# Kernel tuning notes

Hardware: AMD Instinct MI355X
Metric: run time of the kernel (lower is better)

## Reference

```python
import jax, jax.numpy as jnp
import numpy as np

B, H, T = 32, 48, 24
S, A, R, F, L = 256, 64, 8, 1024, 2
EPS = 1e-5


def setup_inputs() -> dict:
    key = jax.random.key(0)
    ks = jax.random.split(key, 12)
    def w(k, shape):
        fan_in = shape[-1]
        return jax.random.normal(k, shape, jnp.float32) / jnp.sqrt(jnp.float32(fan_in))
    return {
        'history_s': jax.random.normal(ks[0], (B, H, S), jnp.float32),
        'history_a': jax.random.normal(ks[1], (B, H, A), jnp.float32),
        'present_s': jax.random.normal(ks[2], (B, S), jnp.float32),
        'future_s': jax.random.normal(ks[3], (B, T, S), jnp.float32),
        'future_a': jax.random.normal(ks[4], (B, T, A), jnp.float32),
        'W_state': w(ks[5], (F, S)), 'b_state': jnp.zeros((F,), jnp.float32),
        'g_sn': jnp.ones((F,), jnp.float32), 'b_sn': jnp.zeros((F,), jnp.float32),
        'W_action': w(ks[6], (F, A)), 'b_action': jnp.zeros((F,), jnp.float32),
        'g_an': jnp.ones((F,), jnp.float32), 'b_an': jnp.zeros((F,), jnp.float32),
        'gru_Wi': w(ks[7], (L, 3 * F, F)), 'gru_Wh': w(ks[8], (L, 3 * F, F)),
        'gru_bi': jnp.zeros((L, 3 * F), jnp.float32), 'gru_bh': jnp.zeros((L, 3 * F), jnp.float32),
        'W_reward': w(ks[9], (R, F)), 'b_reward': jnp.zeros((R,), jnp.float32),
        'W_sout': w(ks[10], (S, F)), 'b_sout': jnp.zeros((S,), jnp.float32),
    }


def _ln(x, g, b):
    m = jnp.mean(x, axis=-1, keepdims=True)
    v = jnp.mean(jnp.square(x - m), axis=-1, keepdims=True)
    return (x - m) / jnp.sqrt(v + EPS) * g + b


def _gelu(x):
    return jax.nn.gelu(x, approximate=False)  # torch F.gelu default = exact erf


def _gru_step(Wi, Wh, bi, bh, hs, x):
    # hs: [L,B,F] hidden per layer; x: [B,F]. PyTorch GRU cell semantics.
    new_hs = []
    inp = x
    for l in range(Wi.shape[0]):
        gi = inp @ Wi[l].T + bi[l]      # [B,3F]
        gh = hs[l] @ Wh[l].T + bh[l]    # [B,3F]
        ir, iz, inn = jnp.split(gi, 3, axis=-1)
        hr, hz, hn = jnp.split(gh, 3, axis=-1)
        r = jax.nn.sigmoid(ir + hr)
        z = jax.nn.sigmoid(iz + hz)
        n = jnp.tanh(inn + r * hn)
        h_new = (1.0 - z) * n + z * hs[l]
        new_hs.append(h_new)
        inp = h_new  # dropout between layers is identity (drop_rate=0)
    return jnp.stack(new_hs), inp


def reference(history_s, history_a, present_s, future_s, future_a,
              W_state, b_state, g_sn, b_sn, W_action, b_action, g_an, b_an,
              gru_Wi, gru_Wh, gru_bi, gru_bh, W_reward, b_reward, W_sout, b_sout):
    # Original forward() reruns the GRU from scratch over a growing window each
    # future step; since h0=0 this is mathematically identical to carrying the
    # hidden state incrementally (module's own _forward variant), which we do.
    Bv = history_s.shape[0]
    Fv = W_state.shape[0]
    Lv = gru_Wi.shape[0]

    hs = _ln(history_s @ W_state.T + b_state, g_sn, b_sn)   # [B,H,F]
    ha = _ln(history_a @ W_action.T + b_action, g_an, b_an)  # [B,H,F]
    ps = _ln(present_s @ W_state.T + b_state, g_sn, b_sn)    # [B,F]
    fa = _ln(future_a @ W_action.T + b_action, g_an, b_an)   # [B,T,F]

    hist_sa = hs + ha  # [B,H,F]

    def head(y):
        r = jnp.tanh(y @ W_reward.T + b_reward)
        s = y @ W_sout.T + b_sout  # state_activation is identity
        return r, s

    # step 0: full window = history + (present + future_a[0])
    seq0 = _gelu(jnp.concatenate([hist_sa, (ps + fa[:, 0])[:, None, :]], axis=1))
    h0 = jnp.zeros((Lv, Bv, Fv), seq0.dtype)

    def scan_seq(h, x):
        h, y = _gru_step(gru_Wi, gru_Wh, gru_bi, gru_bh, h, x)
        return h, y

    hT, ys = jax.lax.scan(scan_seq, h0, jnp.swapaxes(seq0, 0, 1))  # ys: [H+1,B,F]
    r0, s0 = head(ys[-1])
    pres = _ln(s0 @ W_state.T + b_state, g_sn, b_sn)

    def scan_fut(carry, fa_t):
        h, p = carry
        x = _gelu(p + fa_t)  # [B,F]
        h, y = _gru_step(gru_Wi, gru_Wh, gru_bi, gru_bh, h, x)
        r, s = head(y)
        p_new = _ln(s @ W_state.T + b_state, g_sn, b_sn)
        return (h, p_new), (r, s)

    _, (rs, ss) = jax.lax.scan(scan_fut, (hT, pres), jnp.swapaxes(fa[:, 1:], 0, 1))
    future_r = jnp.concatenate([r0[:, None], jnp.swapaxes(rs, 0, 1)], axis=1)  # [B,T,R]
    future_s_out = jnp.concatenate([s0[:, None], jnp.swapaxes(ss, 0, 1)], axis=1)  # [B,T,S]
    return future_r, future_s_out
```

## Files before the change

### kernel.cpp

```cpp
#include <hip/hip_runtime.h>
#include <cmath>

constexpr int kB = 32, kH = 48, kT = 24, kS = 256, kA = 64, kR = 8, kF = 1024;
constexpr int kSEQ = kH + 1;
constexpr float kEPS = 1e-5f;

constexpr int G  = 128;
constexpr int BT = 512;

typedef __attribute__((ext_vector_type(8))) short short8;
typedef __attribute__((ext_vector_type(4))) float f32x4;

union U4S8 { uint4 u; short8 s; };

__device__ __forceinline__ unsigned bfbits(float x) {
  unsigned u = __float_as_uint(x);
  return (u + 0x7fffu + ((u >> 16) & 1u)) >> 16;
}
__device__ __forceinline__ float bf_lo(unsigned u) { return __uint_as_float(u << 16); }
__device__ __forceinline__ float bf_hi(unsigned u) { return __uint_as_float(u & 0xffff0000u); }
__device__ __forceinline__ float bf2f(unsigned short h) {
  return __uint_as_float(((unsigned)h) << 16);
}
__device__ __forceinline__ float gelu_f(float x) {
  return 0.5f * x * (1.0f + erff(x * 0.7071067811865476f));
}
__device__ __forceinline__ float sigmoid_f(float x) {
  return 1.0f / (1.0f + expf(-x));
}

__device__ __forceinline__ void coh_st(unsigned* p, unsigned v) {
  __hip_atomic_store(p, v, __ATOMIC_RELAXED, __HIP_MEMORY_SCOPE_AGENT);
}

__device__ __forceinline__ void sig(unsigned* fl, int grp) {
  if (threadIdx.x == 0)
    __hip_atomic_fetch_add(fl + (grp & 3) * 32, 1u,
                           __ATOMIC_RELAXED, __HIP_MEMORY_SCOPE_AGENT);
}
__device__ __forceinline__ void wait4(const unsigned* fl,
                                      unsigned t0, unsigned t1,
                                      unsigned t2, unsigned t3) {
  if (threadIdx.x == 0) {
    for (;;) {
      unsigned a, b, c, d;
      asm volatile(
        "global_load_dword %0, %4, off sc0 sc1\n\t"
        "global_load_dword %1, %5, off sc0 sc1\n\t"
        "global_load_dword %2, %6, off sc0 sc1\n\t"
        "global_load_dword %3, %7, off sc0 sc1\n\t"
        "s_waitcnt vmcnt(0)"
        : "=&v"(a), "=&v"(b), "=&v"(c), "=&v"(d)
        : "v"(fl), "v"(fl + 32), "v"(fl + 64), "v"(fl + 96)
        : "memory");
      if (a >= t0 && b >= t1 && c >= t2 && d >= t3) break;
    }
  }
  __syncthreads();
}

__device__ __forceinline__ void layer_stage(
    const unsigned short* __restrict__ xsrc,
    const unsigned short* __restrict__ hsrc,
    unsigned short* __restrict__ hdst,
    const short8 (&Bf)[2][3][4],
    float bR, float bZ, float bIN, float bHN,
    float& h_old, float* part, int fb)
{
  const int tid = threadIdx.x;
  const int wv = tid >> 6, l = tid & 63, q = l >> 4, c = l & 15;

  short8 Afr[2][2][4];
  #pragma unroll
  for (int mt = 0; mt < 2; mt++)
    #pragma unroll
    for (int j = 0; j < 4; j++) {
      const int off = (mt*16 + c)*1024 + wv*128 + j*32 + q*8;
      Afr[0][mt][j] = *(const short8*)(xsrc + off);
      Afr[1][mt][j] = *(const short8*)(hsrc + off);
    }

  f32x4 C[4][2];
  #pragma unroll
  for (int s = 0; s < 4; s++)
    #pragma unroll
    for (int mt = 0; mt < 2; mt++)
      C[s][mt] = (f32x4){0.f, 0.f, 0.f, 0.f};

  #pragma unroll
  for (int mt = 0; mt < 2; mt++)
    #pragma unroll
    for (int j = 0; j < 4; j++) {
      C[0][mt] = __builtin_amdgcn_mfma_f32_16x16x32_bf16(Afr[0][mt][j], Bf[0][0][j], C[0][mt], 0, 0, 0);
      C[0][mt] = __builtin_amdgcn_mfma_f32_16x16x32_bf16(Afr[1][mt][j], Bf[1][0][j], C[0][mt], 0, 0, 0);
      C[1][mt] = __builtin_amdgcn_mfma_f32_16x16x32_bf16(Afr[0][mt][j], Bf[0][1][j], C[1][mt], 0, 0, 0);
      C[1][mt] = __builtin_amdgcn_mfma_f32_16x16x32_bf16(Afr[1][mt][j], Bf[1][1][j], C[1][mt], 0, 0, 0);
      C[2][mt] = __builtin_amdgcn_mfma_f32_16x16x32_bf16(Afr[0][mt][j], Bf[0][2][j], C[2][mt], 0, 0, 0);
      C[3][mt] = __builtin_amdgcn_mfma_f32_16x16x32_bf16(Afr[1][mt][j], Bf[1][2][j], C[3][mt], 0, 0, 0);
    }

  const int perm = (wv + l + (l >> 3)) & 7;
  #pragma unroll
  for (int s = 0; s < 4; s++)
    #pragma unroll
    for (int mt = 0; mt < 2; mt++)
      #pragma unroll
      for (int r = 0; r < 4; r++)
        part[((s*2 + mt)*4 + r)*512 + l*8 + perm] = C[s][mt][r];
  __syncthreads();

  const int mt_c = wv & 1, rg = wv >> 1;
  const int b_own = mt_c*16 + q*4 + rg;
  float S[4];
  #pragma unroll
  for (int s = 0; s < 4; s++) {
    const float* pp = part + ((s*2 + mt_c)*4 + rg)*512 + l*8;
    f32x4 a = *(const f32x4*)pp;
    f32x4 b = *(const f32x4*)(pp + 4);
    S[s] = ((a[0]+a[1]) + (a[2]+a[3])) + ((b[0]+b[1]) + (b[2]+b[3]));
  }
  float rr = sigmoid_f(S[0] + bR);
  float zz = sigmoid_f(S[1] + bZ);
  float nn = tanhf(S[2] + bIN + rr * (S[3] + bHN));
  float hn = (1.f - zz)*nn + zz*h_old;
  h_old = hn;
  float nb = __shfl_xor(hn, 1);
  if (!(c & 1)) {
    unsigned pk = bfbits(hn) | (bfbits(nb) << 16);
    coh_st((unsigned*)(hdst + b_own*1024 + fb*16 + c), pk);
  }
  __syncthreads();
}

__device__ __forceinline__ void f3_stage(
    const unsigned short* __restrict__ y_bf, int t,
    const unsigned short* __restrict__ WsT2_bf, const float* __restrict__ b_sout,
    const unsigned short* __restrict__ Wr_bf, const float* __restrict__ b_reward,
    const unsigned short* __restrict__ WstT_bf, const float* __restrict__ b_state,
    const float* __restrict__ g_sn, const float* __restrict__ b_sn,
    const unsigned short* __restrict__ fa_bf,
    float* __restrict__ out_r, float* __restrict__ out_s,
    unsigned short* __restrict__ xbuf_bf, float* part, int b)
{
  const int tid = threadIdx.x;
  float* yb    = part;
  float* spart = part + 1024;
  float* s_sh  = part + 1536;
  float* rpart = part + 1792;
  float* red1  = part + 2048;
  float* red2  = part + 2560;

  {
    unsigned uu = *((const unsigned*)y_bf + b*512 + tid);
    yb[tid*2]     = bf_lo(uu);
    yb[tid*2 + 1] = bf_hi(uu);
  }
  __syncthreads();
  {
    const int j = tid & 255, ksh = tid >> 8;
    const unsigned* wp = (const unsigned*)WsT2_bf + (size_t)ksh*256*256 + j;
    const float* yp = yb + ksh*512;
    float acc = 0.f;
    #pragma unroll 8
    for (int kp = 0; kp < 256; kp++) {
      unsigned w = wp[kp*256];
      acc += bf_lo(w)*yp[2*kp] + bf_hi(w)*yp[2*kp + 1];
    }
    spart[tid] = acc;
  }
  __syncthreads();
  if (tid < 256) {
    float s = spart[tid] + spart[tid + 256] + b_sout[tid];
    out_s[((size_t)b*kT + t)*kS + tid] = s;
    s_sh[tid] = s;
  } else if (tid < 320) {
    const int idx = tid - 256, j = idx >> 3, ks = idx & 7;
    const unsigned short* wr = Wr_bf + j*1024 + ks*128;
    const float* yp = yb + ks*128;
    float acc = 0.f;
    #pragma unroll 4
    for (int k = 0; k < 128; k += 2) {
      unsigned w = *(const unsigned*)(wr + k);
      acc += bf_lo(w)*yp[k] + bf_hi(w)*yp[k+1];
    }
    rpart[idx] = acc;
  }
  __syncthreads();
  if (tid < 8) {
    float a = b_reward[tid];
    #pragma unroll
    for (int ks = 0; ks < 8; ks++) a += rpart[tid*8 + ks];
    out_r[((size_t)b*kT + t)*kR + tid] = tanhf(a);
  }
  if (t == kT - 1) return;
  __syncthreads();
  const int f0 = tid*2;
  float a0 = b_state[f0], a1 = b_state[f0 + 1];
  {
    const unsigned* wp = (const unsigned*)WstT_bf + (f0 >> 1);
    #pragma unroll 8
    for (int k = 0; k < 256; k++) {
      unsigned w = wp[k*512];
      a0 += bf_lo(w)*s_sh[k];
      a1 += bf_hi(w)*s_sh[k];
    }
  }
  float s1 = a0 + a1, s2 = a0*a0 + a1*a1;
  red1[tid] = s1; red2[tid] = s2;
  __syncthreads();
  for (int off = 256; off > 0; off >>= 1) {
    if (tid < off) { red1[tid] += red1[tid + off]; red2[tid] += red2[tid + off]; }
    __syncthreads();
  }
  const float mean = red1[0] * (1.0f/kF);
  const float var  = red2[0] * (1.0f/kF) - mean*mean;
  const float inv  = rsqrtf(var + kEPS);
  unsigned fu = *((const unsigned*)(fa_bf + ((size_t)(t+1)*kB + b)*kF) + tid);
  float x0 = (a0 - mean)*inv*g_sn[f0]   + b_sn[f0]   + bf_lo(fu);
  float x1 = (a1 - mean)*inv*g_sn[f0+1] + b_sn[f0+1] + bf_hi(fu);
  unsigned pk = bfbits(gelu_f(x0)) | (bfbits(gelu_f(x1)) << 16);
  coh_st((unsigned*)xbuf_bf + b*512 + tid, pk);
}

__device__ __forceinline__ void load_bfrags(
    const float* __restrict__ gru_Wi, const float* __restrict__ gru_Wh,
    int lay, int fb, int wv, int q, int c, short8 (&Bf)[2][3][4])
{
  const size_t WLL = (size_t)3 * kF * kF;
  const float* Wm[2] = { gru_Wi + lay*WLL, gru_Wh + lay*WLL };
  #pragma unroll
  for (int m = 0; m < 2; m++)
    #pragma unroll
    for (int g = 0; g < 3; g++)
      #pragma unroll
      for (int j = 0; j < 4; j++) {
        const float* p = Wm[m] + ((size_t)(g*kF + fb*16 + c))*kF + wv*128 + j*32 + q*8;
        float4 a = *(const float4*)p;
        float4 b = *(const float4*)(p + 4);
        U4S8 u;
        u.u.x = bfbits(a.x) | (bfbits(a.y) << 16);
        u.u.y = bfbits(a.z) | (bfbits(a.w) << 16);
        u.u.z = bfbits(b.x) | (bfbits(b.y) << 16);
        u.u.w = bfbits(b.z) | (bfbits(b.w) << 16);
        Bf[m][g][j] = u.s;
      }
}

__global__ __launch_bounds__(BT, 2) void gru_hist(
    const float* __restrict__ gru_Wi, const float* __restrict__ gru_Wh,
    const float* __restrict__ gru_bi, const float* __restrict__ gru_bh,
    const unsigned short* __restrict__ seq0_bf,
    unsigned short* h0pool, unsigned short* h1pool,
    unsigned* hflags)
{
  __shared__ float part[32 * 512];
  const int tid = threadIdx.x;
  const int blk = blockIdx.x;
  const int wv = tid >> 6, l = tid & 63, q = l >> 4, c = l & 15;
  const bool isL1 = (blk >= 64);
  const int fb = blk & 63;
  const int grp = blk >> 4;
  const int lay = isL1 ? 1 : 0;
  const size_t BF = (size_t)kB * kF;

  short8 Bf[2][3][4];
  load_bfrags(gru_Wi, gru_Wh, lay, fb, wv, q, c, Bf);
  const int f = fb*16 + c;
  const float* bi = gru_bi + lay*3*kF;
  const float* bh = gru_bh + lay*3*kF;
  const float bR  = bi[f] + bh[f];
  const float bZ  = bi[kF + f] + bh[kF + f];
  const float bIN = bi[2*kF + f];
  const float bHN = bh[2*kF + f];

  float h_old = 0.f;

  #define H0P(i) (h0pool + (size_t)(i)*BF)
  #define H1P(i) (h1pool + (size_t)(i)*BF)
  #define FH0(s) (hflags + (size_t)((s) - 1) * 128)
  #define FH1(s) (hflags + (size_t)(49 + (s) - 1) * 128)

  for (int s = 0; s < 50; s++) {
    if (!isL1) {
      if (s < 49) {
        if (s >= 1) wait4(FH0(s), 16, 16, 16, 16);
        layer_stage(seq0_bf + (size_t)s*BF, H0P(s), H0P(s+1),
                    Bf, bR, bZ, bIN, bHN, h_old, part, fb);
        sig(FH0(s+1), grp);
      }
    } else {
      if (s >= 1) {
        wait4(FH0(s), 16, 16, 16, 16);
        if (s >= 2) wait4(FH1(s-1), 16, 16, 16, 16);
        layer_stage(H0P(s), H1P(s-1), H1P(s),
                    Bf, bR, bZ, bIN, bHN, h_old, part, fb);
        sig(FH1(s), grp);
      }
    }
  }
  #undef H0P
  #undef H1P
  #undef FH0
  #undef FH1
}

__global__ __launch_bounds__(BT, 2) void gru_fut(
    const float* __restrict__ gru_Wi, const float* __restrict__ gru_Wh,
    const float* __restrict__ gru_bi, const float* __restrict__ gru_bh,
    const unsigned short* __restrict__ WsT2_bf, const float* __restrict__ b_sout,
    const unsigned short* __restrict__ Wr_bf, const float* __restrict__ b_reward,
    const unsigned short* __restrict__ WstT_bf, const float* __restrict__ b_state,
    const float* __restrict__ g_sn, const float* __restrict__ b_sn,
    const unsigned short* __restrict__ fa_bf,
    unsigned short* h0pool, unsigned short* h1pool, unsigned short* xbpool,
    unsigned* fflags,
    float* __restrict__ out_r, float* __restrict__ out_s)
{
  __shared__ float part[32 * 512];
  const int tid = threadIdx.x;
  const int blk = blockIdx.x;
  const int wv = tid >> 6, l = tid & 63, q = l >> 4, c = l & 15;
  const bool isL1 = (blk >= 64);
  const int fb = blk & 63;
  const int grp = blk >> 4;
  const int lay = isL1 ? 1 : 0;
  const size_t BF = (size_t)kB * kF;

  short8 Bf[2][3][4];
  load_bfrags(gru_Wi, gru_Wh, lay, fb, wv, q, c, Bf);
  const int f = fb*16 + c;
  const float* bi = gru_bi + lay*3*kF;
  const float* bh = gru_bh + lay*3*kF;
  const float bR  = bi[f] + bh[f];
  const float bZ  = bi[kF + f] + bh[kF + f];
  const float bIN = bi[2*kF + f];
  const float bHN = bh[2*kF + f];

  #define H0P(i) (h0pool + (size_t)(i)*BF)
  #define H1P(i) (h1pool + (size_t)(i)*BF)
  #define XBP(i) (xbpool + (size_t)(i)*BF)
  #define FXF(t)  (fflags + (size_t)(t) * 128)
  #define FH0F(t) (fflags + (size_t)(23 + (t)) * 128)
  #define FH1F(t) (fflags + (size_t)(46 + (t)) * 128)

  const int b_own = (wv & 1)*16 + q*4 + (wv >> 1);
  float h_old;
  {
    const unsigned short* hs = isL1 ? H1P(49) : H0P(49);
    h_old = bf2f(hs[b_own*1024 + f]);
  }

  for (int t = 0; t < kT; t++) {
    if (blk < kB) {
      if (t >= 1) wait4(FH1F(t-1), 16, 16, 16, 16);
      f3_stage(H1P(49+t), t, WsT2_bf, b_sout, Wr_bf, b_reward,
               WstT_bf, b_state, g_sn, b_sn, fa_bf,
               out_r, out_s, XBP(t), part, blk);
      if (t < kT - 1) { __syncthreads(); sig(FXF(t), grp); }
    }
    if (t == kT - 1) break;
    if (!isL1) {
      wait4(FXF(t), 16, 16, 0, 0);
      if (t >= 1) wait4(FH0F(t-1), 16, 16, 16, 16);
      layer_stage(XBP(t), H0P(49+t), H0P(50+t),
                  Bf, bR, bZ, bIN, bHN, h_old, part, fb);
      sig(FH0F(t), grp);
    } else {
      wait4(FH0F(t), 16, 16, 16, 16);
      if (t >= 1) wait4(FH1F(t-1), 16, 16, 16, 16);
      layer_stage(H0P(50+t), H1P(49+t), H1P(50+t),
                  Bf, bR, bZ, bIN, bHN, h_old, part, fb);
      sig(FH1F(t), grp);
    }
  }
  #undef H0P
  #undef H1P
  #undef XBP
  #undef FXF
  #undef FH0F
  #undef FH1F
}

__global__ __launch_bounds__(512) void convert_weights(
    const float* __restrict__ ws,  unsigned short* __restrict__ wsT2,
    const float* __restrict__ wst, unsigned short* __restrict__ wstT,
    const float* __restrict__ wr,  unsigned short* __restrict__ o3)
{
  const int stride = gridDim.x * blockDim.x;
  const int i0 = blockIdx.x * blockDim.x + threadIdx.x;
  for (int i = i0; i < kS*kF; i += stride) {
    const int j = i >> 10, k = i & 1023;
    wsT2[(k >> 1)*512 + j*2 + (k & 1)] = (unsigned short)bfbits(ws[i]);
  }
  for (int i = i0; i < kF*kS; i += stride) {
    const int ff = i >> 8, k = i & 255;
    wstT[k*1024 + ff] = (unsigned short)bfbits(wst[i]);
  }
  for (int i = i0; i < kR*kF; i += stride) o3[i] = (unsigned short)bfbits(wr[i]);
}

__global__ __launch_bounds__(256) void encode_fa_kernel(
    const float* __restrict__ future_a,
    const float* __restrict__ W_action, const float* __restrict__ b_action,
    const float* __restrict__ g_an, const float* __restrict__ b_an,
    unsigned short* __restrict__ fa_bf)
{
  __shared__ __align__(16) float arow[kA];
  __shared__ float red1[256], red2[256];
  const int bid = blockIdx.x;
  const int b = bid & (kB - 1);
  const int t = bid >> 5;
  const int tid = threadIdx.x;
  if (tid < kA) arow[tid] = future_a[((size_t)b*kT + t)*kA + tid];
  __syncthreads();
  float v[4]; float s1 = 0.f, s2 = 0.f;
  #pragma unroll
  for (int j = 0; j < 4; j++) {
    const int ff = tid + j*256;
    const float* wr = W_action + (size_t)ff*kA;
    float acc = b_action[ff];
    for (int k = 0; k < kA; k += 4) {
      float4 w  = *(const float4*)(wr + k);
      float4 xv = *(const float4*)(arow + k);
      acc += xv.x*w.x + xv.y*w.y + xv.z*w.z + xv.w*w.w;
    }
    v[j] = acc; s1 += acc; s2 += acc*acc;
  }
  red1[tid] = s1; red2[tid] = s2;
  __syncthreads();
  for (int off = 128; off > 0; off >>= 1) {
    if (tid < off) { red1[tid] += red1[tid+off]; red2[tid] += red2[tid+off]; }
    __syncthreads();
  }
  const float m = red1[0] * (1.0f/kF);
  const float va = red2[0] * (1.0f/kF) - m*m;
  const float inv = rsqrtf(va + kEPS);
  #pragma unroll
  for (int j = 0; j < 4; j++) {
    const int ff = tid + j*256;
    fa_bf[((size_t)t*kB + b)*kF + ff] =
        (unsigned short)bfbits((v[j] - m)*inv*g_an[ff] + b_an[ff]);
  }
}

__global__ __launch_bounds__(256) void encode_seq0_kernel(
    const float* __restrict__ history_s, const float* __restrict__ history_a,
    const float* __restrict__ present_s,
    const float* __restrict__ W_state, const float* __restrict__ b_state,
    const float* __restrict__ g_sn, const float* __restrict__ b_sn,
    const float* __restrict__ W_action, const float* __restrict__ b_action,
    const float* __restrict__ g_an, const float* __restrict__ b_an,
    const unsigned short* __restrict__ fa_bf, unsigned short* __restrict__ seq0_bf)
{
  __shared__ __align__(16) float srow[kS];
  __shared__ __align__(16) float arow[kA];
  __shared__ float red1[256], red2[256];
  const int bid = blockIdx.x;
  const int b = bid & (kB - 1);
  const int t = bid >> 5;
  const int tid = threadIdx.x;
  const bool hist = (t < kH);
  const float* sp = hist ? (history_s + ((size_t)b*kH + t)*kS)
                         : (present_s + (size_t)b*kS);
  srow[tid] = sp[tid];
  if (hist && tid < kA) arow[tid] = history_a[((size_t)b*kH + t)*kA + tid];
  __syncthreads();

  float u[4]; float s1 = 0.f, s2 = 0.f;
  #pragma unroll
  for (int j = 0; j < 4; j++) {
    const int ff = tid + j*256;
    const float* wr = W_state + (size_t)ff*kS;
    float acc = b_state[ff];
    for (int k = 0; k < kS; k += 4) {
      float4 w  = *(const float4*)(wr + k);
      float4 xv = *(const float4*)(srow + k);
      acc += xv.x*w.x + xv.y*w.y + xv.z*w.z + xv.w*w.w;
    }
    u[j] = acc; s1 += acc; s2 += acc*acc;
  }
  red1[tid] = s1; red2[tid] = s2;
  __syncthreads();
  for (int off = 128; off > 0; off >>= 1) {
    if (tid < off) { red1[tid] += red1[tid+off]; red2[tid] += red2[tid+off]; }
    __syncthreads();
  }
  const float mu = red1[0] * (1.0f/kF);
  const float vu = red2[0] * (1.0f/kF) - mu*mu;
  const float iu = rsqrtf(vu + kEPS);
  __syncthreads();

  if (hist) {
    float v[4]; s1 = 0.f; s2 = 0.f;
    #pragma unroll
    for (int j = 0; j < 4; j++) {
      const int ff = tid + j*256;
      const float* wr = W_action + (size_t)ff*kA;
      float acc = b_action[ff];
      for (int k = 0; k < kA; k += 4) {
        float4 w  = *(const float4*)(wr + k);
        float4 xv = *(const float4*)(arow + k);
        acc += xv.x*w.x + xv.y*w.y + xv.z*w.z + xv.w*w.w;
      }
      v[j] = acc; s1 += acc; s2 += acc*acc;
    }
    red1[tid] = s1; red2[tid] = s2;
    __syncthreads();
    for (int off = 128; off > 0; off >>= 1) {
      if (tid < off) { red1[tid] += red1[tid+off]; red2[tid] += red2[tid+off]; }
      __syncthreads();
    }
    const float mv = red1[0] * (1.0f/kF);
    const float vv = red2[0] * (1.0f/kF) - mv*mv;
    const float iv = rsqrtf(vv + kEPS);
    #pragma unroll
    for (int j = 0; j < 4; j++) {
      const int ff = tid + j*256;
      const float un = (u[j] - mu)*iu*g_sn[ff] + b_sn[ff];
      const float vn = (v[j] - mv)*iv*g_an[ff] + b_an[ff];
      seq0_bf[((size_t)t*kB + b)*kF + ff] = (unsigned short)bfbits(gelu_f(un + vn));
    }
  } else {
    #pragma unroll
    for (int j = 0; j < 4; j++) {
      const int ff = tid + j*256;
      const float un = (u[j] - mu)*iu*g_sn[ff] + b_sn[ff];
      seq0_bf[((size_t)t*kB + b)*kF + ff] =
          (unsigned short)bfbits(gelu_f(un + bf2f(fa_bf[(size_t)b*kF + ff])));
    }
  }
}

extern "C" void kernel_launch(void* const* d_in, const int* in_sizes, int n_in,
                              void* d_out, int out_size, void* d_ws, size_t ws_size,
                              hipStream_t stream) {
  (void)in_sizes; (void)n_in; (void)out_size;
  const float* history_s = (const float*)d_in[0];
  const float* history_a = (const float*)d_in[1];
  const float* present_s = (const float*)d_in[2];
  const float* future_a  = (const float*)d_in[4];
  const float* W_state   = (const float*)d_in[5];
  const float* b_state   = (const float*)d_in[6];
  const float* g_sn      = (const float*)d_in[7];
  const float* b_sn      = (const float*)d_in[8];
  const float* W_action  = (const float*)d_in[9];
  const float* b_action  = (const float*)d_in[10];
  const float* g_an      = (const float*)d_in[11];
  const float* b_an      = (const float*)d_in[12];
  const float* gru_Wi    = (const float*)d_in[13];
  const float* gru_Wh    = (const float*)d_in[14];
  const float* gru_bi    = (const float*)d_in[15];
  const float* gru_bh    = (const float*)d_in[16];
  const float* W_reward  = (const float*)d_in[17];
  const float* b_reward  = (const float*)d_in[18];
  const float* W_sout    = (const float*)d_in[19];
  const float* b_sout    = (const float*)d_in[20];

  char* ws = (char*)d_ws;
  unsigned short* seq0_bf = (unsigned short*)(ws + 0);
  unsigned short* fa_bf   = (unsigned short*)(ws + 3211264);
  unsigned short* WsT2_bf = (unsigned short*)(ws + 4784128);
  unsigned short* WstT_bf = (unsigned short*)(ws + 5308416);
  unsigned short* Wr_bf   = (unsigned short*)(ws + 5832704);
  unsigned short* h0pool  = (unsigned short*)(ws + 5849088);
  unsigned short* h1pool  = (unsigned short*)(ws + 10633216);
  unsigned short* xbpool  = (unsigned short*)(ws + 15417344);
  unsigned*       hflags  = (unsigned*)(ws + 16924672);
  unsigned*       fflags  = (unsigned*)(ws + 16974848);
  const size_t need = 17010176;
  if (ws_size < need) return;

  hipMemsetAsync((void*)h0pool, 0, 65536, stream);
  hipMemsetAsync((void*)h1pool, 0, 65536, stream);
  hipMemsetAsync((void*)hflags, 0, 50176 + 35328, stream);

  float* out_r = (float*)d_out;
  float* out_s = out_r + (size_t)kB*kT*kR;

  hipLaunchKernelGGL(convert_weights, dim3(256), dim3(512), 0, stream,
                     W_sout, WsT2_bf, W_state, WstT_bf, W_reward, Wr_bf);
  hipLaunchKernelGGL(encode_fa_kernel, dim3(kT*kB), dim3(256), 0, stream,
                     future_a, W_action, b_action, g_an, b_an, fa_bf);
  hipLaunchKernelGGL(encode_seq0_kernel, dim3(kSEQ*kB), dim3(256), 0, stream,
                     history_s, history_a, present_s,
                     W_state, b_state, g_sn, b_sn,
                     W_action, b_action, g_an, b_an, fa_bf, seq0_bf);
  hipLaunchKernelGGL(gru_hist, dim3(G), dim3(BT), 0, stream,
                     gru_Wi, gru_Wh, gru_bi, gru_bh,
                     seq0_bf, h0pool, h1pool, hflags);
  hipLaunchKernelGGL(gru_fut, dim3(G), dim3(BT), 0, stream,
                     gru_Wi, gru_Wh, gru_bi, gru_bh,
                     WsT2_bf, b_sout, Wr_bf, b_reward, WstT_bf, b_state,
                     g_sn, b_sn, fa_bf,
                     h0pool, h1pool, xbpool, fflags,
                     out_r, out_s);
}
```

Measured before the change: 1.582 ms.

## Use finer-grained per-wave dependency flags and overlap x loads with h waits

Replaces the coarse block-wide wait4 barriers before each GRU layer stage with per-octet counters. Each wave waits only on the flag line covering the 128-column slice of h it reads, and loads x (or h) before waiting on the other operand, so part of the memory latency overlaps the dependency wait. Adds s_sleep in the spin loops and enlarges the flag region. This trades more atomics and flag lines for less serialization across the persistent-kernel pipeline, at the risk of heavier polling traffic or subtle ordering bugs.

Result: faster. 1.472 ms (-7.0%).

```diff
diff --git a/kernel.cpp b/kernel.cpp
--- a/kernel.cpp
+++ b/kernel.cpp
@@ -33,10 +33,15 @@
   __hip_atomic_store(p, v, __ATOMIC_RELAXED, __HIP_MEMORY_SCOPE_AGENT);
 }
 
-__device__ __forceinline__ void sig(unsigned* fl, int grp) {
-  if (threadIdx.x == 0)
-    __hip_atomic_fetch_add(fl + (grp & 3) * 32, 1u,
-                           __ATOMIC_RELAXED, __HIP_MEMORY_SCOPE_AGENT);
+__device__ __forceinline__ void wwait(const unsigned* line, unsigned tgt) {
+  for (;;) {
+    unsigned v;
+    asm volatile("global_load_dword %0, %1, off sc0 sc1\n\t"
+                 "s_waitcnt vmcnt(0)"
+                 : "=v"(v) : "v"(line) : "memory");
+    if (v >= tgt) break;
+    __builtin_amdgcn_s_sleep(1);
+  }
 }
 __device__ __forceinline__ void wait4(const unsigned* fl,
                                       unsigned t0, unsigned t1,
@@ -54,15 +59,30 @@
         : "v"(fl), "v"(fl + 32), "v"(fl + 64), "v"(fl + 96)
         : "memory");
       if (a >= t0 && b >= t1 && c >= t2 && d >= t3) break;
-    }
-  }
-  __syncthreads();
+      __builtin_amdgcn_s_sleep(1);
+    }
+  }
+  __syncthreads();
+}
+__device__ __forceinline__ void sig_oct(unsigned* fl, int fb) {
+  if (threadIdx.x == 0)
+    __hip_atomic_fetch_add(fl + ((fb >> 3) & 7) * 32, 1u,
+                           __ATOMIC_RELAXED, __HIP_MEMORY_SCOPE_AGENT);
+}
+__device__ __forceinline__ void sig16(unsigned* fl, int b) {
+  if (threadIdx.x == 0)
+    __hip_atomic_fetch_add(fl + ((b >> 4) & 1) * 32, 1u,
+                           __ATOMIC_RELAXED, __HIP_MEMORY_SCOPE_AGENT);
 }
 
 __device__ __forceinline__ void layer_stage(
     const unsigned short* __restrict__ xsrc,
     const unsigned short* __restrict__ hsrc,
     unsigned short* __restrict__ hdst,
+    const unsigned* xw8,
+    const unsigned* hw8,
+    const unsigned* xblk2,
+    int hfirst,
     const short8 (&Bf)[2][3][4],
     float bR, float bZ, float bIN, float bHN,
     float& h_old, float* part, int fb)
@@ -70,15 +90,36 @@
   const int tid = threadIdx.x;
   const int wv = tid >> 6, l = tid & 63, q = l >> 4, c = l & 15;
 
-  short8 Afr[2][2][4];
-  #pragma unroll
-  for (int mt = 0; mt < 2; mt++)
-    #pragma unroll
-    for (int j = 0; j < 4; j++) {
-      const int off = (mt*16 + c)*1024 + wv*128 + j*32 + q*8;
-      Afr[0][mt][j] = *(const short8*)(xsrc + off);
-      Afr[1][mt][j] = *(const short8*)(hsrc + off);
-    }
+  short8 Ax[2][4], Ah[2][4];
+  const int base = c*1024 + wv*128 + q*8;
+
+  if (hfirst) {
+    if (hw8) wwait(hw8 + wv*32, 8u);
+    #pragma unroll
+    for (int mt = 0; mt < 2; mt++)
+      #pragma unroll
+      for (int j = 0; j < 4; j++)
+        Ah[mt][j] = *(const short8*)(hsrc + base + mt*16*1024 + j*32);
+    if (xblk2) wait4(xblk2, 16u, 16u, 0u, 0u);
+    if (xw8) wwait(xw8 + wv*32, 8u);
+    #pragma unroll
+    for (int mt = 0; mt < 2; mt++)
+      #pragma unroll
+      for (int j = 0; j < 4; j++)
+        Ax[mt][j] = *(const short8*)(xsrc + base + mt*16*1024 + j*32);
+  } else {
+    #pragma unroll
+    for (int mt = 0; mt < 2; mt++)
+      #pragma unroll
+      for (int j = 0; j < 4; j++)
+        Ax[mt][j] = *(const short8*)(xsrc + base + mt*16*1024 + j*32);
+    if (hw8) wwait(hw8 + wv*32, 8u);
+    #pragma unroll
+    for (int mt = 0; mt < 2; mt++)
+      #pragma unroll
+      for (int j = 0; j < 4; j++)
+        Ah[mt][j] = *(const short8*)(hsrc + base + mt*16*1024 + j*32);
+  }
 
   f32x4 C[4][2];
   #pragma unroll
@@ -91,12 +132,12 @@
   for (int mt = 0; mt < 2; mt++)
     #pragma unroll
     for (int j = 0; j < 4; j++) {
-      C[0][mt] = __builtin_amdgcn_mfma_f32_16x16x32_bf16(Afr[0][mt][j], Bf[0][0][j], C[0][mt], 0, 0, 0);
-      C[0][mt] = __builtin_amdgcn_mfma_f32_16x16x32_bf16(Afr[1][mt][j], Bf[1][0][j], C[0][mt], 0, 0, 0);
-      C[1][mt] = __builtin_amdgcn_mfma_f32_16x16x32_bf16(Afr[0][mt][j], Bf[0][1][j], C[1][mt], 0, 0, 0);
-      C[1][mt] = __builtin_amdgcn_mfma_f32_16x16x32_bf16(Afr[1][mt][j], Bf[1][1][j], C[1][mt], 0, 0, 0);
-      C[2][mt] = __builtin_amdgcn_mfma_f32_16x16x32_bf16(Afr[0][mt][j], Bf[0][2][j], C[2][mt], 0, 0, 0);
-      C[3][mt] = __builtin_amdgcn_mfma_f32_16x16x32_bf16(Afr[1][mt][j], Bf[1][2][j], C[3][mt], 0, 0, 0);
+      C[0][mt] = __builtin_amdgcn_mfma_f32_16x16x32_bf16(Ax[mt][j], Bf[0][0][j], C[0][mt], 0, 0, 0);
+      C[0][mt] = __builtin_amdgcn_mfma_f32_16x16x32_bf16(Ah[mt][j], Bf[1][0][j], C[0][mt], 0, 0, 0);
+      C[1][mt] = __builtin_amdgcn_mfma_f32_16x16x32_bf16(Ax[mt][j], Bf[0][1][j], C[1][mt], 0, 0, 0);
+      C[1][mt] = __builtin_amdgcn_mfma_f32_16x16x32_bf16(Ah[mt][j], Bf[1][1][j], C[1][mt], 0, 0, 0);
+      C[2][mt] = __builtin_amdgcn_mfma_f32_16x16x32_bf16(Ax[mt][j], Bf[0][2][j], C[2][mt], 0, 0, 0);
+      C[3][mt] = __builtin_amdgcn_mfma_f32_16x16x32_bf16(Ah[mt][j], Bf[1][2][j], C[3][mt], 0, 0, 0);
     }
 
   const int perm = (wv + l + (l >> 3)) & 7;
@@ -259,7 +300,6 @@
   const int wv = tid >> 6, l = tid & 63, q = l >> 4, c = l & 15;
   const bool isL1 = (blk >= 64);
   const int fb = blk & 63;
-  const int grp = blk >> 4;
   const int lay = isL1 ? 1 : 0;
   const size_t BF = (size_t)kB * kF;
 
@@ -277,24 +317,23 @@
 
   #define H0P(i) (h0pool + (size_t)(i)*BF)
   #define H1P(i) (h1pool + (size_t)(i)*BF)
-  #define FH0(s) (hflags + (size_t)((s) - 1) * 128)
-  #define FH1(s) (hflags + (size_t)(49 + (s) - 1) * 128)
+  #define FH0(s) (hflags + (size_t)((s) - 1) * 256)
+  #define FH1(s) (hflags + (size_t)(48 + (s)) * 256)
 
   for (int s = 0; s < 50; s++) {
     if (!isL1) {
       if (s < 49) {
-        if (s >= 1) wait4(FH0(s), 16, 16, 16, 16);
         layer_stage(seq0_bf + (size_t)s*BF, H0P(s), H0P(s+1),
+                    nullptr, (s >= 1) ? FH0(s) : nullptr, nullptr, 0,
                     Bf, bR, bZ, bIN, bHN, h_old, part, fb);
-        sig(FH0(s+1), grp);
+        sig_oct(FH0(s+1), fb);
       }
     } else {
       if (s >= 1) {
-        wait4(FH0(s), 16, 16, 16, 16);
-        if (s >= 2) wait4(FH1(s-1), 16, 16, 16, 16);
         layer_stage(H0P(s), H1P(s-1), H1P(s),
+                    FH0(s), (s >= 2) ? FH1(s-1) : nullptr, nullptr, 1,
                     Bf, bR, bZ, bIN, bHN, h_old, part, fb);
-        sig(FH1(s), grp);
+        sig_oct(FH1(s), fb);
       }
     }
   }
@@ -322,7 +361,6 @@
   const int wv = tid >> 6, l = tid & 63, q = l >> 4, c = l & 15;
   const bool isL1 = (blk >= 64);
   const int fb = blk & 63;
-  const int grp = blk >> 4;
   const int lay = isL1 ? 1 : 0;
   const size_t BF = (size_t)kB * kF;
 
@@ -339,9 +377,9 @@
   #define H0P(i) (h0pool + (size_t)(i)*BF)
   #define H1P(i) (h1pool + (size_t)(i)*BF)
   #define XBP(i) (xbpool + (size_t)(i)*BF)
-  #define FXF(t)  (fflags + (size_t)(t) * 128)
-  #define FH0F(t) (fflags + (size_t)(23 + (t)) * 128)
-  #define FH1F(t) (fflags + (size_t)(46 + (t)) * 128)
+  #define FH0F(t) (fflags + (size_t)(t) * 256)
+  #define FH1F(t) (fflags + (size_t)(23 + (t)) * 256)
+  #define FXF(t)  (fflags + (size_t)46 * 256 + (size_t)(t) * 64)
 
   const int b_own = (wv & 1)*16 + q*4 + (wv >> 1);
   float h_old;
@@ -352,33 +390,34 @@
 
   for (int t = 0; t < kT; t++) {
     if (blk < kB) {
-      if (t >= 1) wait4(FH1F(t-1), 16, 16, 16, 16);
+      if (t >= 1) {
+        wait4(FH1F(t-1), 8u, 8u, 8u, 8u);
+        wait4(FH1F(t-1) + 128, 8u, 8u, 8u, 8u);
+      }
       f3_stage(H1P(49+t), t, WsT2_bf, b_sout, Wr_bf, b_reward,
                WstT_bf, b_state, g_sn, b_sn, fa_bf,
                out_r, out_s, XBP(t), part, blk);
-      if (t < kT - 1) { __syncthreads(); sig(FXF(t), grp); }
+      if (t < kT - 1) { __syncthreads(); sig16(FXF(t), blk); }
     }
     if (t == kT - 1) break;
     if (!isL1) {
-      wait4(FXF(t), 16, 16, 0, 0);
-      if (t >= 1) wait4(FH0F(t-1), 16, 16, 16, 16);
       layer_stage(XBP(t), H0P(49+t), H0P(50+t),
+                  nullptr, (t >= 1) ? FH0F(t-1) : nullptr, FXF(t), 1,
                   Bf, bR, bZ, bIN, bHN, h_old, part, fb);
-      sig(FH0F(t), grp);
+      sig_oct(FH0F(t), fb);
     } else {
-      wait4(FH0F(t), 16, 16, 16, 16);
-      if (t >= 1) wait4(FH1F(t-1), 16, 16, 16, 16);
       layer_stage(H0P(50+t), H1P(49+t), H1P(50+t),
+                  FH0F(t), (t >= 1) ? FH1F(t-1) : nullptr, nullptr, 1,
                   Bf, bR, bZ, bIN, bHN, h_old, part, fb);
-      sig(FH1F(t), grp);
+      sig_oct(FH1F(t), fb);
     }
   }
   #undef H0P
   #undef H1P
   #undef XBP
-  #undef FXF
   #undef FH0F
   #undef FH1F
+  #undef FXF
 }
 
 __global__ __launch_bounds__(512) void convert_weights(
@@ -566,13 +605,13 @@
   unsigned short* h1pool  = (unsigned short*)(ws + 10633216);
   unsigned short* xbpool  = (unsigned short*)(ws + 15417344);
   unsigned*       hflags  = (unsigned*)(ws + 16924672);
-  unsigned*       fflags  = (unsigned*)(ws + 16974848);
-  const size_t need = 17010176;
+  unsigned*       fflags  = (unsigned*)(ws + 17025024);
+  const size_t need = 17078016;
   if (ws_size < need) return;
 
   hipMemsetAsync((void*)h0pool, 0, 65536, stream);
   hipMemsetAsync((void*)h1pool, 0, 65536, stream);
-  hipMemsetAsync((void*)hflags, 0, 50176 + 35328, stream);
+  hipMemsetAsync((void*)hflags, 0, 100352 + 52992, stream);
 
   float* out_r = (float*)d_out;
   float* out_s = out_r + (size_t)kB*kT*kR;
```
